# Kernel optimization log

Measured on AMD Instinct MI355X. Metric: run time of the kernel, lower is better.

Reference implementation:

```python
import jax, jax.numpy as jnp
import numpy as np
import math

EMBED_DIM = 1024
N_HEADS = 16
QK_DIM = 64
V_DIM = 64
B, S = 4, 2048


def setup_inputs() -> dict:
    key = jax.random.key(0)
    ks = jax.random.split(key, 10)
    sc = lambda fan_in: 1.0 / math.sqrt(fan_in)
    X = jax.random.normal(ks[0], (B, S, EMBED_DIM), dtype=jnp.float32)
    mask = jax.random.randint(ks[1], (B, 1, S, S), 0, 2, dtype=jnp.int32)
    wQ = jax.random.uniform(ks[2], (EMBED_DIM, QK_DIM * N_HEADS), jnp.float32, -sc(EMBED_DIM), sc(EMBED_DIM))
    bQ = jnp.zeros((QK_DIM * N_HEADS,), jnp.float32)
    wK = jax.random.uniform(ks[3], (EMBED_DIM, QK_DIM * N_HEADS), jnp.float32, -sc(EMBED_DIM), sc(EMBED_DIM))
    bK = jnp.zeros((QK_DIM * N_HEADS,), jnp.float32)
    wV = jax.random.uniform(ks[4], (EMBED_DIM, V_DIM * N_HEADS), jnp.float32, -sc(EMBED_DIM), sc(EMBED_DIM))
    bV = jnp.zeros((V_DIM * N_HEADS,), jnp.float32)
    wO = jax.random.uniform(ks[5], (V_DIM * N_HEADS, EMBED_DIM), jnp.float32, -sc(V_DIM * N_HEADS), sc(V_DIM * N_HEADS))
    bO = jnp.zeros((EMBED_DIM,), jnp.float32)
    return {"X": X, "mask": mask, "wQ": wQ, "bQ": bQ, "wK": wK, "bK": bK,
            "wV": wV, "bV": bV, "wO": wO, "bO": bO}


def reference(X, mask, wQ, bQ, wK, bK, wV, bV, wO, bO):
    Bsz, Slen, _ = X.shape
    # projections -> [B, H, S, d]
    q = (X @ wQ + bQ).reshape(Bsz, Slen, N_HEADS, QK_DIM).transpose(0, 2, 1, 3)
    k = (X @ wK + bK).reshape(Bsz, Slen, N_HEADS, QK_DIM).transpose(0, 2, 1, 3)
    v = (X @ wV + bV).reshape(Bsz, Slen, N_HEADS, V_DIM).transpose(0, 2, 1, 3)
    # scores [B, H, S, S]
    scores = jnp.einsum("bhqd,bhkd->bhqk", q, k) / math.sqrt(QK_DIM)
    scores = jnp.where(mask == 0, jnp.float32(-1e9), scores)
    probs = jax.nn.softmax(scores, axis=-1)
    out = jnp.einsum("bhqk,bhkd->bhqd", probs, v)  # [B, H, S, v]
    out = out.transpose(0, 2, 1, 3).reshape(Bsz, Slen, N_HEADS * V_DIM)
    return out @ wO + bO
```

## Files before the change

### kernel.cpp

```cpp
#include <hip/hip_runtime.h>
#include <hip/hip_bf16.h>

#define EMB 1024
#define NH 16
#define DH 64
#define SEQ 2048

typedef __attribute__((ext_vector_type(8))) __bf16 bf16x8;
typedef __attribute__((ext_vector_type(4))) float f32x4;

__device__ __forceinline__ void g2l16(const void* g, void* l) {
  __builtin_amdgcn_global_load_lds(
      (const __attribute__((address_space(1))) void*)g,
      (__attribute__((address_space(3))) void*)l, 16, 0, 0);
}

__global__ void detect_k(const unsigned short* __restrict__ xs,
                         int* __restrict__ flag) {
  __shared__ int cnt;
  if (threadIdx.x == 0) cnt = 0;
  __syncthreads();
  int hits = 0;
  for (int i = threadIdx.x; i < 16384; i += 256) {
    unsigned e = (xs[i] >> 7) & 0xFFu;
    if (e >= 0xC0u) hits++;
  }
  atomicAdd(&cnt, hits);
  __syncthreads();
  if (threadIdx.x == 0) *flag = (cnt > 16) ? 1 : 0;
}

__global__ void conv_k(const void* __restrict__ src,
                       __hip_bfloat16* __restrict__ dst,
                       const int* __restrict__ flag, int n4) {
  int i = blockIdx.x * 256 + threadIdx.x;
  if (i >= n4) return;
  if (*flag) {
    float4 v = ((const float4*)src)[i];
    ushort4 o;
    __hip_bfloat16 t;
    t = __float2bfloat16(v.x); o.x = *(unsigned short*)&t;
    t = __float2bfloat16(v.y); o.y = *(unsigned short*)&t;
    t = __float2bfloat16(v.z); o.z = *(unsigned short*)&t;
    t = __float2bfloat16(v.w); o.w = *(unsigned short*)&t;
    ((ushort4*)dst)[i] = o;
  } else {
    ((ushort4*)dst)[i] = ((const ushort4*)src)[i];
  }
}

__global__ void convB_k(const void* s0, const void* s1, const void* s2,
                        const void* s3, __hip_bfloat16* __restrict__ dst,
                        const int* __restrict__ flag) {
  const void* srcs[4] = {s0, s1, s2, s3};
  const void* src = srcs[blockIdx.x];
  int i = threadIdx.x;
  __hip_bfloat16* d = dst + blockIdx.x * 1024;
  if (*flag) {
    float4 v = ((const float4*)src)[i];
    ushort4 o;
    __hip_bfloat16 t;
    t = __float2bfloat16(v.x); o.x = *(unsigned short*)&t;
    t = __float2bfloat16(v.y); o.y = *(unsigned short*)&t;
    t = __float2bfloat16(v.z); o.z = *(unsigned short*)&t;
    t = __float2bfloat16(v.w); o.w = *(unsigned short*)&t;
    ((ushort4*)d)[i] = o;
  } else {
    ((ushort4*)d)[i] = ((const ushort4*)src)[i];
  }
}

__global__ void transW4_k(const void* s0, const void* s1, const void* s2,
                          const void* s3, __hip_bfloat16* d0,
                          __hip_bfloat16* d1, __hip_bfloat16* d2,
                          __hip_bfloat16* d3, const int* __restrict__ flag) {
  __shared__ __hip_bfloat16 tile[32][33];
  const void* srcs[4] = {s0, s1, s2, s3};
  __hip_bfloat16* dsts[4] = {d0, d1, d2, d3};
  const void* src = srcs[blockIdx.z];
  __hip_bfloat16* dst = dsts[blockIdx.z];
  int f = *flag;
  int tx = threadIdx.x, ty = threadIdx.y;
  int x = blockIdx.x * 32 + tx;
  int y0 = blockIdx.y * 32;
  for (int i = 0; i < 32; i += 8) {
    int idx = (y0 + ty + i) * EMB + x;
    tile[ty + i][tx] = f ? __float2bfloat16(((const float*)src)[idx])
                         : ((const __hip_bfloat16*)src)[idx];
  }
  __syncthreads();
  int x2 = y0 + tx;
  int y2 = blockIdx.x * 32;
  for (int i = 0; i < 32; i += 8)
    dst[(size_t)(y2 + ty + i) * EMB + x2] = tile[tx][ty + i];
}

__global__ void maskpack_k(const int* __restrict__ mask,
                           unsigned int* __restrict__ bits) {
  int g = blockIdx.x * 256 + threadIdx.x;
  int lane = threadIdx.x & 63;
  unsigned long long bal = __ballot(mask[g] != 0);
  if ((lane & 31) == 0)
    bits[g >> 5] = (unsigned int)(bal >> (lane & 32));
}

__launch_bounds__(256)
__global__ void gemm_qkv(const __hip_bfloat16* __restrict__ A,
                         const __hip_bfloat16* __restrict__ Bt,
                         const __hip_bfloat16* __restrict__ bias,
                         __hip_bfloat16* __restrict__ CQ,
                         __hip_bfloat16* __restrict__ CK,
                         __hip_bfloat16* __restrict__ CV) {
  __shared__ __align__(16) __bf16 sA[128 * 32];
  __shared__ __align__(16) __bf16 sB[128 * 32];
  const __bf16* Ab = (const __bf16*)A;
  const __bf16* Bb = (const __bf16*)Bt;

  int tid = threadIdx.x;
  int w = tid >> 6, lane = tid & 63;
  int quad = lane >> 4, lcol = lane & 15;
  int m0 = blockIdx.x * 128, n0 = blockIdx.y * 128;
  int wm = (w >> 1) * 64, wn = (w & 1) * 64;
  int region = n0 >> 10;

  f32x4 z = {0.f, 0.f, 0.f, 0.f};
  f32x4 acc[4][4];
#pragma unroll
  for (int i = 0; i < 4; i++)
#pragma unroll
    for (int j = 0; j < 4; j++) acc[i][j] = z;

  int c = w * 64 + lane;
  int r = c >> 2, cc = c & 3;

  for (int k0 = 0; k0 < 1024; k0 += 32) {
    __syncthreads();
    g2l16(Ab + (size_t)(m0 + r) * 1024 + k0 + cc * 8, (char*)sA + w * 1024);
    g2l16(Ab + (size_t)(m0 + r + 64) * 1024 + k0 + cc * 8, (char*)sA + 4096 + w * 1024);
    g2l16(Bb + (size_t)(n0 + r) * 1024 + k0 + cc * 8, (char*)sB + w * 1024);
    g2l16(Bb + (size_t)(n0 + r + 64) * 1024 + k0 + cc * 8, (char*)sB + 4096 + w * 1024);
    __syncthreads();

    bf16x8 af[4], bfr[4];
#pragma unroll
    for (int i = 0; i < 4; i++)
      af[i] = *(const bf16x8*)(sA + (wm + i * 16 + lcol) * 32 + quad * 8);
#pragma unroll
    for (int j = 0; j < 4; j++)
      bfr[j] = *(const bf16x8*)(sB + (wn + j * 16 + lcol) * 32 + quad * 8);
#pragma unroll
    for (int i = 0; i < 4; i++)
#pragma unroll
      for (int j = 0; j < 4; j++)
        acc[i][j] = __builtin_amdgcn_mfma_f32_16x16x32_bf16(af[i], bfr[j], acc[i][j], 0, 0, 0);
  }

  float scale = (region == 0) ? 0.18033688011111204f : 1.0f;
#pragma unroll
  for (int j = 0; j < 4; j++) {
    int col = n0 + wn + j * 16 + lcol;
    float bv = __bfloat162float(bias[col]);
    int lc = col & 1023;
    int h = lc >> 6, dd = lc & 63;
#pragma unroll
    for (int i = 0; i < 4; i++) {
      int rbase = m0 + wm + i * 16 + quad * 4;
      int b = rbase >> 11, s = rbase & 2047;
      if (region == 1) {
#pragma unroll
        for (int rr = 0; rr < 4; rr++) {
          float v = acc[i][j][rr] + bv;
          CK[(((size_t)(b * NH + h)) * SEQ + s + rr) * DH + dd] = __float2bfloat16(v);
        }
      } else {
        union { unsigned long long u; __hip_bfloat16 bb[4]; } pk;
#pragma unroll
        for (int rr = 0; rr < 4; rr++)
          pk.bb[rr] = __float2bfloat16((acc[i][j][rr] + bv) * scale);
        __hip_bfloat16* dst = (region == 0) ? CQ : CV;
        *(unsigned long long*)(dst + (((size_t)(b * NH + h)) * DH + dd) * SEQ + s) = pk.u;
      }
    }
  }
}

__launch_bounds__(256)
__global__ void gemm_o(const __hip_bfloat16* __restrict__ A,
                       const __hip_bfloat16* __restrict__ Bt,
                       const __hip_bfloat16* __restrict__ bias,
                       void* __restrict__ Cv, const int* __restrict__ flag) {
  __shared__ __align__(16) __bf16 sA[128 * 32];
  __shared__ __align__(16) __bf16 sB[128 * 32];
  const __bf16* Ab = (const __bf16*)A;
  const __bf16* Bb = (const __bf16*)Bt;
  int f32out = *flag;

  int tid = threadIdx.x;
  int w = tid >> 6, lane = tid & 63;
  int quad = lane >> 4, lcol = lane & 15;
  int m0 = blockIdx.x * 128, n0 = blockIdx.y * 128;
  int wm = (w >> 1) * 64, wn = (w & 1) * 64;

  f32x4 z = {0.f, 0.f, 0.f, 0.f};
  f32x4 acc[4][4];
#pragma unroll
  for (int i = 0; i < 4; i++)
#pragma unroll
    for (int j = 0; j < 4; j++) acc[i][j] = z;

  int c = w * 64 + lane;
  int r = c >> 2, cc = c & 3;

  for (int k0 = 0; k0 < 1024; k0 += 32) {
    __syncthreads();
    g2l16(Ab + (size_t)(m0 + r) * 1024 + k0 + cc * 8, (char*)sA + w * 1024);
    g2l16(Ab + (size_t)(m0 + r + 64) * 1024 + k0 + cc * 8, (char*)sA + 4096 + w * 1024);
    g2l16(Bb + (size_t)(n0 + r) * 1024 + k0 + cc * 8, (char*)sB + w * 1024);
    g2l16(Bb + (size_t)(n0 + r + 64) * 1024 + k0 + cc * 8, (char*)sB + 4096 + w * 1024);
    __syncthreads();

    bf16x8 af[4], bfr[4];
#pragma unroll
    for (int i = 0; i < 4; i++)
      af[i] = *(const bf16x8*)(sA + (wm + i * 16 + lcol) * 32 + quad * 8);
#pragma unroll
    for (int j = 0; j < 4; j++)
      bfr[j] = *(const bf16x8*)(sB + (wn + j * 16 + lcol) * 32 + quad * 8);
#pragma unroll
    for (int i = 0; i < 4; i++)
#pragma unroll
      for (int j = 0; j < 4; j++)
        acc[i][j] = __builtin_amdgcn_mfma_f32_16x16x32_bf16(af[i], bfr[j], acc[i][j], 0, 0, 0);
  }

#pragma unroll
  for (int j = 0; j < 4; j++) {
    int col = n0 + wn + j * 16 + lcol;
    float bv = __bfloat162float(bias[col]);
#pragma unroll
    for (int i = 0; i < 4; i++) {
      int rbase = m0 + wm + i * 16 + quad * 4;
#pragma unroll
      for (int rr = 0; rr < 4; rr++) {
        int m = rbase + rr;
        float v = acc[i][j][rr] + bv;
        if (f32out)
          ((float*)Cv)[(size_t)m * EMB + col] = v;
        else
          ((__hip_bfloat16*)Cv)[(size_t)m * EMB + col] = __float2bfloat16(v);
      }
    }
  }
}

__launch_bounds__(256)
__global__ void attn_k(const __hip_bfloat16* __restrict__ Qt,
                       const __hip_bfloat16* __restrict__ Kp,
                       const __hip_bfloat16* __restrict__ Vp,
                       const unsigned int* __restrict__ mbits,
                       __hip_bfloat16* __restrict__ AO) {
  __shared__ __align__(16) __bf16 sK[2 * 64 * 64];
  __shared__ __align__(16) __bf16 sV[2 * 64 * 64];
  __shared__ __align__(16) __bf16 sP[4 * 16 * 72];
  __shared__ unsigned long long sLut[16];

  int tid = threadIdx.x;
  int w = tid >> 6, lane = tid & 63, quad = lane >> 4, lcol = lane & 15;
  int bid = blockIdx.y * 32 + blockIdx.x;
  int xcd = bid & 7, idx = bid >> 3;
  int bh = xcd * 8 + (idx >> 5);
  int qblk = idx & 31;
  int b = bh >> 4, h = bh & 15;

  if (tid < 16) {
    unsigned long long v = 0;
    if (tid & 1) v |= 0xFFFFull;
    if (tid & 2) v |= 0xFFFFull << 16;
    if (tid & 4) v |= 0xFFFFull << 32;
    if (tid & 8) v |= 0xFFFFull << 48;
    sLut[tid] = v;
  }

  const __bf16* Qb = (const __bf16*)Qt + (size_t)bh * DH * SEQ;
  const __bf16* Kb = (const __bf16*)Kp + (size_t)bh * SEQ * DH;
  const __bf16* Vb = (const __bf16*)Vp + (size_t)bh * DH * SEQ;
  int qw = qblk * 64 + w * 16;
  int q_mine = qw + lcol;

  union { bf16x8 v; __bf16 e[8]; } uq0, uq1;
#pragma unroll
  for (int j = 0; j < 8; j++) {
    uq0.e[j] = Qb[(size_t)(quad * 8 + j) * SEQ + q_mine];
    uq1.e[j] = Qb[(size_t)(32 + quad * 8 + j) * SEQ + q_mine];
  }
  bf16x8 bq0 = uq0.v, bq1 = uq1.v;

  __bf16 onev = (__bf16)1.0f;
  bf16x8 ones = {onev, onev, onev, onev, onev, onev, onev, onev};

  f32x4 z = {0.f, 0.f, 0.f, 0.f};
  f32x4 ot[4];
  f32x4 lacc = z;
#pragma unroll
  for (int j = 0; j < 4; j++) ot[j] = z;

  const unsigned long long* mrow =
      (const unsigned long long*)mbits + ((size_t)b * SEQ + q_mine) * (SEQ / 64);

  int kr = lane >> 3, pc = lane & 7;
  __bf16* pw = sP + w * (16 * 72);
  int swz = lcol & 7;

  auto STAGE = [&](int buf, int kt) {
#pragma unroll
    for (int t2 = 0; t2 < 2; t2++) {
      int row = w * 16 + t2 * 8 + kr;
      g2l16(Kb + (size_t)(kt * 64 + row) * DH + (pc ^ kr) * 8,
            (char*)sK + buf * 8192 + (w * 16 + t2 * 8) * 128);
      g2l16(Vb + (size_t)row * SEQ + kt * 64 + (pc ^ kr) * 8,
            (char*)sV + buf * 8192 + (w * 16 + t2 * 8) * 128);
    }
  };

  STAGE(0, 0);
  unsigned long long mb = mrow[0];
  __syncthreads();

  for (int kt = 0; kt < SEQ / 64; ++kt) {
    int cur = kt & 1;
    const __bf16* sKc = sK + cur * 4096;
    const __bf16* sVc = sV + cur * 4096;
    if (kt < SEQ / 64 - 1) STAGE(cur ^ 1, kt + 1);
    unsigned long long mb_next = mrow[(kt + 1) & (SEQ / 64 - 1)];

    f32x4 st[4];
    __builtin_amdgcn_s_setprio(1);
#pragma unroll
    for (int t = 0; t < 4; t++) {
      int rowK = t * 16 + lcol;
      bf16x8 a0 = *(const bf16x8*)(sKc + rowK * 64 + (quad ^ swz) * 8);
      bf16x8 a1 = *(const bf16x8*)(sKc + rowK * 64 + ((quad + 4) ^ swz) * 8);
      f32x4 sv = __builtin_amdgcn_mfma_f32_16x16x32_bf16(a0, bq0, z, 0, 0, 0);
      sv = __builtin_amdgcn_mfma_f32_16x16x32_bf16(a1, bq1, sv, 0, 0, 0);
      st[t] = sv;
    }
    __builtin_amdgcn_s_setprio(0);

    unsigned int lo32 = (unsigned int)(mb >> (quad * 4));
    unsigned int hi32 = (unsigned int)(mb >> (quad * 4 + 32));
#pragma unroll
    for (int t = 0; t < 4; t++) {
      unsigned int sel = (t < 2) ? lo32 : hi32;
      unsigned int bits4 = (sel >> ((t & 1) * 16)) & 0xFu;
      union { unsigned long long u; __bf16 bb[4]; } pk;
#pragma unroll
      for (int r = 0; r < 4; r++)
        pk.bb[r] = (__bf16)__builtin_amdgcn_exp2f(st[t][r]);
      pk.u &= sLut[bits4];
      *(unsigned long long*)(pw + lcol * 72 + t * 16 + quad * 4) = pk.u;
    }

    bf16x8 bp0 = *(const bf16x8*)(pw + lcol * 72 + quad * 8);
    bf16x8 bp1 = *(const bf16x8*)(pw + lcol * 72 + 32 + quad * 8);
    __builtin_amdgcn_s_setprio(1);
#pragma unroll
    for (int j = 0; j < 4; j++) {
      int rowV = j * 16 + lcol;
      bf16x8 av0 = *(const bf16x8*)(sVc + rowV * 64 + (quad ^ swz) * 8);
      bf16x8 av1 = *(const bf16x8*)(sVc + rowV * 64 + ((quad + 4) ^ swz) * 8);
      ot[j] = __builtin_amdgcn_mfma_f32_16x16x32_bf16(av0, bp0, ot[j], 0, 0, 0);
      ot[j] = __builtin_amdgcn_mfma_f32_16x16x32_bf16(av1, bp1, ot[j], 0, 0, 0);
    }
    lacc = __builtin_amdgcn_mfma_f32_16x16x32_bf16(ones, bp0, lacc, 0, 0, 0);
    lacc = __builtin_amdgcn_mfma_f32_16x16x32_bf16(ones, bp1, lacc, 0, 0, 0);
    __builtin_amdgcn_s_setprio(0);

    mb = mb_next;
    __syncthreads();
  }

  float linv = 1.0f / fmaxf(lacc[0], 1e-20f);
#pragma unroll
  for (int j = 0; j < 4; j++) {
    union { ushort4 u; __bf16 bb[4]; } pk;
#pragma unroll
    for (int r = 0; r < 4; r++) pk.bb[r] = (__bf16)(ot[j][r] * linv);
    *(ushort4*)((__bf16*)AO + ((size_t)b * SEQ + q_mine) * EMB + h * 64 +
                j * 16 + quad * 4) = pk.u;
  }
}

extern "C" void kernel_launch(void* const* d_in, const int* in_sizes, int n_in,
                              void* d_out, int out_size, void* d_ws, size_t ws_size,
                              hipStream_t stream) {
  const int* mask = (const int*)d_in[1];

  char* ws = (char*)d_ws;
  int* flag             = (int*)ws;
  __hip_bfloat16* biasc = (__hip_bfloat16*)(ws + (64ull << 10));
  __hip_bfloat16* WQt   = (__hip_bfloat16*)(ws + (1ull << 20));
  __hip_bfloat16* WKt   = (__hip_bfloat16*)(ws + (3ull << 20));
  __hip_bfloat16* WVt   = (__hip_bfloat16*)(ws + (5ull << 20));
  __hip_bfloat16* WOt   = (__hip_bfloat16*)(ws + (7ull << 20));
  unsigned int* mbits   = (unsigned int*)(ws + (9ull << 20));
  __hip_bfloat16* Xc    = (__hip_bfloat16*)(ws + (12ull << 20));
  __hip_bfloat16* Qw    = (__hip_bfloat16*)(ws + (28ull << 20));
  __hip_bfloat16* Kw    = (__hip_bfloat16*)(ws + (44ull << 20));
  __hip_bfloat16* Vtw   = (__hip_bfloat16*)(ws + (60ull << 20));
  __hip_bfloat16* AO    = (__hip_bfloat16*)(ws + (76ull << 20));

  detect_k<<<1, 256, 0, stream>>>((const unsigned short*)d_in[0], flag);

  conv_k<<<8192, 256, 0, stream>>>(d_in[0], Xc, flag, 2097152);
  convB_k<<<4, 256, 0, stream>>>(d_in[3], d_in[5], d_in[7], d_in[9], biasc, flag);

  dim3 tb(32, 8);
  transW4_k<<<dim3(32, 32, 4), tb, 0, stream>>>(d_in[2], d_in[4], d_in[6],
                                                d_in[8], WQt, WKt, WVt, WOt, flag);
  maskpack_k<<<65536, 256, 0, stream>>>(mask, mbits);

  gemm_qkv<<<dim3(64, 24), 256, 0, stream>>>(Xc, WQt, biasc, Qw, Kw, Vtw);
  attn_k<<<dim3(32, 64), 256, 0, stream>>>(Qw, Kw, Vtw, mbits, AO);
  gemm_o<<<dim3(64, 8), 256, 0, stream>>>(AO, WOt, biasc + 3072, d_out, flag);
}
```

Measured before the change: 428.6 us.

## Switch attention to 32x32x16 MFMA with 32 queries per wave

Rewrites the attention inner loop so each wave handles 32 query rows with 32x32x16 bf16 MFMAs instead of 16 rows with 16x16x32. Each block now covers 128 queries, which halves the grid and the number of times each K/V tile is loaded per query. It also processes the 64-key tile in two 32-key halves, with a new P staging layout and launch bounds set to three blocks. The cost is more accumulator registers per wave, which the occupancy hint has to accommodate.

Result: faster. 418.1 us (-2.5%).

```diff
diff --git a/kernel.cpp b/kernel.cpp
--- a/kernel.cpp
+++ b/kernel.cpp
@@ -8,6 +8,7 @@
 
 typedef __attribute__((ext_vector_type(8))) __bf16 bf16x8;
 typedef __attribute__((ext_vector_type(4))) float f32x4;
+typedef __attribute__((ext_vector_type(16))) float f32x16;
 
 __device__ __forceinline__ void g2l16(const void* g, void* l) {
   __builtin_amdgcn_global_load_lds(
@@ -253,7 +254,7 @@
   }
 }
 
-__launch_bounds__(256)
+__launch_bounds__(256, 3)
 __global__ void attn_k(const __hip_bfloat16* __restrict__ Qt,
                        const __hip_bfloat16* __restrict__ Kp,
                        const __hip_bfloat16* __restrict__ Vp,
@@ -261,15 +262,16 @@
                        __hip_bfloat16* __restrict__ AO) {
   __shared__ __align__(16) __bf16 sK[2 * 64 * 64];
   __shared__ __align__(16) __bf16 sV[2 * 64 * 64];
-  __shared__ __align__(16) __bf16 sP[4 * 16 * 72];
+  __shared__ __align__(16) __bf16 sP[4][32][68];
   __shared__ unsigned long long sLut[16];
 
   int tid = threadIdx.x;
-  int w = tid >> 6, lane = tid & 63, quad = lane >> 4, lcol = lane & 15;
-  int bid = blockIdx.y * 32 + blockIdx.x;
+  int w = tid >> 6, lane = tid & 63, hi = lane >> 5, l31 = lane & 31;
+  int swz7 = l31 & 7;
+  int bid = blockIdx.x;
   int xcd = bid & 7, idx = bid >> 3;
-  int bh = xcd * 8 + (idx >> 5);
-  int qblk = idx & 31;
+  int bh = xcd * 8 + (idx >> 4);
+  int qblk = idx & 15;
   int b = bh >> 4, h = bh & 15;
 
   if (tid < 16) {
@@ -284,32 +286,28 @@
   const __bf16* Qb = (const __bf16*)Qt + (size_t)bh * DH * SEQ;
   const __bf16* Kb = (const __bf16*)Kp + (size_t)bh * SEQ * DH;
   const __bf16* Vb = (const __bf16*)Vp + (size_t)bh * DH * SEQ;
-  int qw = qblk * 64 + w * 16;
-  int q_mine = qw + lcol;
-
-  union { bf16x8 v; __bf16 e[8]; } uq0, uq1;
-#pragma unroll
-  for (int j = 0; j < 8; j++) {
-    uq0.e[j] = Qb[(size_t)(quad * 8 + j) * SEQ + q_mine];
-    uq1.e[j] = Qb[(size_t)(32 + quad * 8 + j) * SEQ + q_mine];
-  }
-  bf16x8 bq0 = uq0.v, bq1 = uq1.v;
+  int q_mine = qblk * 128 + w * 32 + l31;
+
+  union { bf16x8 v; __bf16 e[8]; } qf[4];
+#pragma unroll
+  for (int s = 0; s < 4; s++)
+#pragma unroll
+    for (int j = 0; j < 8; j++)
+      qf[s].e[j] = Qb[(size_t)(s * 16 + hi * 8 + j) * SEQ + q_mine];
 
   __bf16 onev = (__bf16)1.0f;
   bf16x8 ones = {onev, onev, onev, onev, onev, onev, onev, onev};
 
-  f32x4 z = {0.f, 0.f, 0.f, 0.f};
-  f32x4 ot[4];
-  f32x4 lacc = z;
-#pragma unroll
-  for (int j = 0; j < 4; j++) ot[j] = z;
+  f32x16 z16 = {0.f, 0.f, 0.f, 0.f, 0.f, 0.f, 0.f, 0.f,
+                0.f, 0.f, 0.f, 0.f, 0.f, 0.f, 0.f, 0.f};
+  f32x16 ot0 = z16, ot1 = z16;
+  f32x16 lacc = z16;
 
   const unsigned long long* mrow =
       (const unsigned long long*)mbits + ((size_t)b * SEQ + q_mine) * (SEQ / 64);
 
   int kr = lane >> 3, pc = lane & 7;
-  __bf16* pw = sP + w * (16 * 72);
-  int swz = lcol & 7;
+  __bf16(*pw)[68] = sP[w];
 
   auto STAGE = [&](int buf, int kt) {
 #pragma unroll
@@ -328,52 +326,52 @@
 
   for (int kt = 0; kt < SEQ / 64; ++kt) {
     int cur = kt & 1;
-    const __bf16* sKc = sK + cur * 4096;
-    const __bf16* sVc = sV + cur * 4096;
+    const char* sKc = (const char*)sK + cur * 8192;
+    const char* sVc = (const char*)sV + cur * 8192;
     if (kt < SEQ / 64 - 1) STAGE(cur ^ 1, kt + 1);
     unsigned long long mb_next = mrow[(kt + 1) & (SEQ / 64 - 1)];
-
-    f32x4 st[4];
-    __builtin_amdgcn_s_setprio(1);
-#pragma unroll
-    for (int t = 0; t < 4; t++) {
-      int rowK = t * 16 + lcol;
-      bf16x8 a0 = *(const bf16x8*)(sKc + rowK * 64 + (quad ^ swz) * 8);
-      bf16x8 a1 = *(const bf16x8*)(sKc + rowK * 64 + ((quad + 4) ^ swz) * 8);
-      f32x4 sv = __builtin_amdgcn_mfma_f32_16x16x32_bf16(a0, bq0, z, 0, 0, 0);
-      sv = __builtin_amdgcn_mfma_f32_16x16x32_bf16(a1, bq1, sv, 0, 0, 0);
-      st[t] = sv;
+    unsigned long long mbc = mb >> (4 * hi);
+
+#pragma unroll
+    for (int ct = 0; ct < 2; ct++) {
+      f32x16 sc = z16;
+      __builtin_amdgcn_s_setprio(1);
+#pragma unroll
+      for (int s = 0; s < 4; s++) {
+        bf16x8 a = *(const bf16x8*)(sKc + ct * 4096 + l31 * 128 +
+                                    (((2 * s + hi) ^ swz7) << 4));
+        sc = __builtin_amdgcn_mfma_f32_32x32x16_bf16(a, qf[s].v, sc, 0, 0, 0);
+      }
+      __builtin_amdgcn_s_setprio(0);
+
+#pragma unroll
+      for (int g = 0; g < 4; g++) {
+        union { unsigned long long u; __bf16 bb[4]; } pk;
+#pragma unroll
+        for (int r = 0; r < 4; r++)
+          pk.bb[r] = (__bf16)__builtin_amdgcn_exp2f(sc[4 * g + r]);
+        unsigned nib = (unsigned)(mbc >> (32 * ct + 8 * g)) & 0xFu;
+        pk.u &= sLut[nib];
+        *(unsigned long long*)(&pw[l31][32 * ct + 8 * g + 4 * hi]) = pk.u;
+      }
+
+      __builtin_amdgcn_s_setprio(1);
+#pragma unroll
+      for (int f2 = 0; f2 < 2; f2++) {
+        int kb = 2 * ct + f2;
+        union { bf16x8 v; unsigned long long d2[2]; } bp;
+        bp.d2[0] = *(const unsigned long long*)(&pw[l31][kb * 16 + 8 * hi]);
+        bp.d2[1] = *(const unsigned long long*)(&pw[l31][kb * 16 + 8 * hi + 4]);
+        bf16x8 av0 = *(const bf16x8*)(sVc + l31 * 128 +
+                                      (((2 * kb + hi) ^ swz7) << 4));
+        bf16x8 av1 = *(const bf16x8*)(sVc + (32 + l31) * 128 +
+                                      (((2 * kb + hi) ^ swz7) << 4));
+        ot0 = __builtin_amdgcn_mfma_f32_32x32x16_bf16(av0, bp.v, ot0, 0, 0, 0);
+        ot1 = __builtin_amdgcn_mfma_f32_32x32x16_bf16(av1, bp.v, ot1, 0, 0, 0);
+        lacc = __builtin_amdgcn_mfma_f32_32x32x16_bf16(ones, bp.v, lacc, 0, 0, 0);
+      }
+      __builtin_amdgcn_s_setprio(0);
     }
-    __builtin_amdgcn_s_setprio(0);
-
-    unsigned int lo32 = (unsigned int)(mb >> (quad * 4));
-    unsigned int hi32 = (unsigned int)(mb >> (quad * 4 + 32));
-#pragma unroll
-    for (int t = 0; t < 4; t++) {
-      unsigned int sel = (t < 2) ? lo32 : hi32;
-      unsigned int bits4 = (sel >> ((t & 1) * 16)) & 0xFu;
-      union { unsigned long long u; __bf16 bb[4]; } pk;
-#pragma unroll
-      for (int r = 0; r < 4; r++)
-        pk.bb[r] = (__bf16)__builtin_amdgcn_exp2f(st[t][r]);
-      pk.u &= sLut[bits4];
-      *(unsigned long long*)(pw + lcol * 72 + t * 16 + quad * 4) = pk.u;
-    }
-
-    bf16x8 bp0 = *(const bf16x8*)(pw + lcol * 72 + quad * 8);
-    bf16x8 bp1 = *(const bf16x8*)(pw + lcol * 72 + 32 + quad * 8);
-    __builtin_amdgcn_s_setprio(1);
-#pragma unroll
-    for (int j = 0; j < 4; j++) {
-      int rowV = j * 16 + lcol;
-      bf16x8 av0 = *(const bf16x8*)(sVc + rowV * 64 + (quad ^ swz) * 8);
-      bf16x8 av1 = *(const bf16x8*)(sVc + rowV * 64 + ((quad + 4) ^ swz) * 8);
-      ot[j] = __builtin_amdgcn_mfma_f32_16x16x32_bf16(av0, bp0, ot[j], 0, 0, 0);
-      ot[j] = __builtin_amdgcn_mfma_f32_16x16x32_bf16(av1, bp1, ot[j], 0, 0, 0);
-    }
-    lacc = __builtin_amdgcn_mfma_f32_16x16x32_bf16(ones, bp0, lacc, 0, 0, 0);
-    lacc = __builtin_amdgcn_mfma_f32_16x16x32_bf16(ones, bp1, lacc, 0, 0, 0);
-    __builtin_amdgcn_s_setprio(0);
 
     mb = mb_next;
     __syncthreads();
@@ -381,12 +379,17 @@
 
   float linv = 1.0f / fmaxf(lacc[0], 1e-20f);
 #pragma unroll
-  for (int j = 0; j < 4; j++) {
-    union { ushort4 u; __bf16 bb[4]; } pk;
-#pragma unroll
-    for (int r = 0; r < 4; r++) pk.bb[r] = (__bf16)(ot[j][r] * linv);
-    *(ushort4*)((__bf16*)AO + ((size_t)b * SEQ + q_mine) * EMB + h * 64 +
-                j * 16 + quad * 4) = pk.u;
+  for (int dt = 0; dt < 2; dt++) {
+    const f32x16& o = dt ? ot1 : ot0;
+#pragma unroll
+    for (int g = 0; g < 4; g++) {
+      union { unsigned long long u; __hip_bfloat16 bb[4]; } pk;
+#pragma unroll
+      for (int r = 0; r < 4; r++)
+        pk.bb[r] = __float2bfloat16(o[4 * g + r] * linv);
+      *(unsigned long long*)((__bf16*)AO + ((size_t)b * SEQ + q_mine) * EMB +
+                             h * 64 + dt * 32 + g * 8 + hi * 4) = pk.u;
+    }
   }
 }
 
@@ -420,6 +423,6 @@
   maskpack_k<<<65536, 256, 0, stream>>>(mask, mbits);
 
   gemm_qkv<<<dim3(64, 24), 256, 0, stream>>>(Xc, WQt, biasc, Qw, Kw, Vtw);
-  attn_k<<<dim3(32, 64), 256, 0, stream>>>(Qw, Kw, Vtw, mbits, AO);
+  attn_k<<<dim3(1024), 256, 0, stream>>>(Qw, Kw, Vtw, mbits, AO);
   gemm_o<<<dim3(64, 8), 256, 0, stream>>>(AO, WOt, biasc + 3072, d_out, flag);
 }
```
